# Performance work log

Measured on AMD Instinct MI355X. Metric: run time of the kernel, lower is better.

Reference implementation:

```python
import jax, jax.numpy as jnp
import numpy as np

ROW_PENALTY = 10.0
SENTINEL = 9999.0
T_DIM, D_DIM = 4096, 1024
MASK_DENSITY = 0.7


def setup_inputs() -> dict:
    key = jax.random.key(0)
    k1, k2, k3, k4 = jax.random.split(key, 4)
    X = jax.random.normal(k1, (T_DIM, D_DIM), dtype=jnp.float32)
    H = jax.random.normal(k2, (T_DIM, D_DIM), dtype=jnp.float32)
    C = jax.random.normal(k3, (T_DIM, D_DIM), dtype=jnp.float32)
    # binary observation mask (the torch code treats M as 0/1: M[i]*M[j] > 0)
    M = (jax.random.uniform(k4, (T_DIM, D_DIM)) < MASK_DENSITY).astype(jnp.float32)
    return {"X": X, "H": H, "C": C, "M": M, "T": T_DIM}


def reference(X, H, C, M, T):
    # Binary mask (values already 0/1); M[i]*M[j] > 0  <=>  Mb[i]*Mb[j] == 1.
    Mb = (M > 0).astype(H.dtype)                      # [T, D]
    MH = Mb * H                                       # masked first moment terms
    MH2 = MH * H                                      # masked second moment terms

    # Pairwise masked-variance of (H[i] - H[j]) over dims where both masks are on,
    # expressed exactly as GEMMs (no [T,T,D] intermediate):
    n = Mb @ Mb.T                                     # [T,T] overlap counts
    s1 = MH @ Mb.T - Mb @ MH.T                        # sum_d w * (H_i - H_j)
    s2 = MH2 @ Mb.T - 2.0 * (MH @ MH.T) + Mb @ MH2.T  # sum_d w * (H_i - H_j)^2

    nsafe = jnp.maximum(n, 2.0)
    var = (s2 - s1 * s1 / nsafe) / (nsafe - 1.0)      # unbiased, like torch.var

    am = jnp.argmin(M, axis=1)                        # first-min index per row
    eye = jnp.eye(T, dtype=bool)
    valid = (am[:, None] != am[None, :]) & (~eye) & (n > 1.5)
    scores = jnp.where(valid, var, SENTINEL)          # torch inits scores to 9999

    min_row = jnp.argmin(scores, axis=1)              # [T]
    row_loss = jnp.sum(jnp.linalg.norm(H - H[min_row], axis=1))

    mse = jnp.sum(((X - (H - C)) * M) ** 2)           # MSELoss(reduction='sum') of X*M vs (H-C)*M
    return mse + ROW_PENALTY * row_loss
```

## Files before the change

### kernel.cpp

```cpp
#include <hip/hip_runtime.h>
#include <stdint.h>

#define TD 4096
#define DD 1024
#define SENT 9999.0f

typedef __attribute__((ext_vector_type(4))) float f32x4;
typedef __attribute__((ext_vector_type(8))) short short8;
typedef __attribute__((ext_vector_type(4))) unsigned short ushort4v;

__device__ __forceinline__ unsigned short f2bf(float f) {
  union { float f; unsigned int u; } v; v.f = f;
  unsigned int u = v.u;
  return (unsigned short)((u + 0x7FFFu + ((u >> 16) & 1u)) >> 16);
}

__device__ __forceinline__ void gld_lds16(const void* g, void* l) {
  __builtin_amdgcn_global_load_lds(
      (const __attribute__((address_space(1))) unsigned int*)(size_t)g,
      (__attribute__((address_space(3))) unsigned int*)(unsigned int)(size_t)l,
      16, 0, 0);
}

__global__ __launch_bounds__(256) void k_init(unsigned long long* row_min, float* out) {
  int i = blockIdx.x * 256 + threadIdx.x;
  if (i < TD) row_min[i] = ~0ull;
  if (i == 0) out[0] = 0.0f;
}

__global__ __launch_bounds__(256) void k_prep(
    const float* __restrict__ X, const float* __restrict__ H,
    const float* __restrict__ C, const float* __restrict__ M,
    unsigned short* __restrict__ Mbh, unsigned short* __restrict__ MHh,
    unsigned short* __restrict__ MH2h, int* __restrict__ am,
    float* __restrict__ out)
{
  const int row = blockIdx.x;
  const int tid = threadIdx.x;
  const size_t base = (size_t)row * DD;
  f32x4 x = ((const f32x4*)(X + base))[tid];
  f32x4 h = ((const f32x4*)(H + base))[tid];
  f32x4 c = ((const f32x4*)(C + base))[tid];
  f32x4 m = ((const f32x4*)(M + base))[tid];
  float mse = 0.0f;
  int cand = 0x7FFFFFFF;
  ushort4v mb, mh, mh2;
#pragma unroll
  for (int e = 0; e < 4; ++e) {
    float mv = m[e], hv = h[e];
    float mbv = (mv > 0.0f) ? 1.0f : 0.0f;
    float mhv = mbv * hv;
    float mh2v = mhv * hv;
    mb[e] = f2bf(mbv);
    mh[e] = f2bf(mhv);
    mh2[e] = f2bf(mh2v);
    float t = (x[e] - (hv - c[e])) * mv;
    mse += t * t;
    int d = tid * 4 + e;
    if (mv == 0.0f && d < cand) cand = d;
  }
  *(ushort4v*)(Mbh + base + tid * 4) = mb;
  *(ushort4v*)(MHh + base + tid * 4) = mh;
  *(ushort4v*)(MH2h + base + tid * 4) = mh2;
#pragma unroll
  for (int o = 32; o > 0; o >>= 1) {
    mse += __shfl_down(mse, o);
    int oc = __shfl_down(cand, o);
    cand = (oc < cand) ? oc : cand;
  }
  __shared__ float rs[4];
  __shared__ int ri[4];
  if ((tid & 63) == 0) { rs[tid >> 6] = mse; ri[tid >> 6] = cand; }
  __syncthreads();
  if (tid == 0) {
    float s = rs[0] + rs[1] + rs[2] + rs[3];
    int cm = ri[0];
    cm = (ri[1] < cm) ? ri[1] : cm;
    cm = (ri[2] < cm) ? ri[2] : cm;
    cm = (ri[3] < cm) ? ri[3] : cm;
    atomicAdd(out, s);
    am[row] = (cm == 0x7FFFFFFF) ? 0 : cm;
  }
}

__global__ __launch_bounds__(256, 3) void k_pairvar(
    const unsigned short* __restrict__ Mb, const unsigned short* __restrict__ MH,
    const unsigned short* __restrict__ MH2, const int* __restrict__ am,
    unsigned long long* __restrict__ row_min)
{
  __shared__ unsigned short lds[6 * 64 * 64];
  const int tid = threadIdx.x;
  const int lane = tid & 63;
  const int w = tid >> 6;
  const int wr = w >> 1, wc = w & 1;

  const int kblk = blockIdx.x;
  int bi = (int)((sqrtf(8.0f * (float)kblk + 1.0f) - 1.0f) * 0.5f);
  while ((bi + 1) * (bi + 2) / 2 <= kblk) ++bi;
  while (bi * (bi + 1) / 2 > kblk) --bi;
  const int bj = kblk - bi * (bi + 1) / 2;
  const int i0 = bi * 64, j0 = bj * 64;

  const unsigned short* mats[3] = { Mb, MH, MH2 };
  const int l_row = lane >> 3;
  const int l_ch = lane & 7;
  const int sw_ch = l_ch ^ l_row;

  const unsigned short* gsrc[12];
  unsigned int ldsoff[12];
#pragma unroll
  for (int s = 0; s < 12; ++s) {
    int t = w * 12 + s;
    int tile = t >> 3;
    int rowblk = t & 7;
    int mat = (tile < 3) ? tile : (tile - 3);
    int rbase = (tile < 3) ? i0 : j0;
    int grow = rbase + rowblk * 8 + l_row;
    gsrc[s] = mats[mat] + (size_t)grow * DD + sw_ch * 8;
    ldsoff[s] = (unsigned int)((tile * 4096 + rowblk * 512) * 2);
  }

  f32x4 acc[6][2][2] = {};

  for (int kt = 0; kt < DD / 64; ++kt) {
#pragma unroll
    for (int s = 0; s < 12; ++s)
      gld_lds16(gsrc[s] + kt * 64, (char*)lds + ldsoff[s]);
    __syncthreads();
#pragma unroll
    for (int kc = 0; kc < 2; ++kc) {
      short8 aF[3][2], bF[3][2];
      const int ksub = kc * 4 + (lane >> 4);
#pragma unroll
      for (int m = 0; m < 2; ++m) {
        const int r = wr * 32 + m * 16 + (lane & 15);
        const int sl = ksub ^ (r & 7);
#pragma unroll
        for (int mat = 0; mat < 3; ++mat)
          aF[mat][m] = *(const short8*)&lds[mat * 4096 + r * 64 + sl * 8];
      }
#pragma unroll
      for (int n = 0; n < 2; ++n) {
        const int r = wc * 32 + n * 16 + (lane & 15);
        const int sl = ksub ^ (r & 7);
#pragma unroll
        for (int mat = 0; mat < 3; ++mat)
          bF[mat][n] = *(const short8*)&lds[(3 + mat) * 4096 + r * 64 + sl * 8];
      }
#pragma unroll
      for (int m = 0; m < 2; ++m)
#pragma unroll
        for (int n = 0; n < 2; ++n) {
          acc[0][m][n] = __builtin_amdgcn_mfma_f32_16x16x32_bf16(aF[0][m], bF[0][n], acc[0][m][n], 0, 0, 0);
          acc[1][m][n] = __builtin_amdgcn_mfma_f32_16x16x32_bf16(aF[1][m], bF[0][n], acc[1][m][n], 0, 0, 0);
          acc[2][m][n] = __builtin_amdgcn_mfma_f32_16x16x32_bf16(aF[0][m], bF[1][n], acc[2][m][n], 0, 0, 0);
          acc[3][m][n] = __builtin_amdgcn_mfma_f32_16x16x32_bf16(aF[2][m], bF[0][n], acc[3][m][n], 0, 0, 0);
          acc[4][m][n] = __builtin_amdgcn_mfma_f32_16x16x32_bf16(aF[0][m], bF[2][n], acc[4][m][n], 0, 0, 0);
          acc[5][m][n] = __builtin_amdgcn_mfma_f32_16x16x32_bf16(aF[1][m], bF[1][n], acc[5][m][n], 0, 0, 0);
        }
    }
    __syncthreads();
  }

  const int cl = lane & 15;
  const int lg = lane >> 4;
  int amj[2];
#pragma unroll
  for (int n = 0; n < 2; ++n) amj[n] = am[j0 + wc * 32 + n * 16 + cl];

  unsigned long long bestc[2] = { ~0ull, ~0ull };

#pragma unroll
  for (int m = 0; m < 2; ++m) {
#pragma unroll
    for (int q = 0; q < 4; ++q) {
      const int gi = i0 + wr * 32 + m * 16 + lg * 4 + q;
      const int ami = am[gi];
      unsigned long long best = ~0ull;
#pragma unroll
      for (int n = 0; n < 2; ++n) {
        const int gj = j0 + wc * 32 + n * 16 + cl;
        const float nv = acc[0][m][n][q];
        const float bb = acc[1][m][n][q];
        const float bt = acc[2][m][n][q];
        const float cc = acc[3][m][n][q];
        const float ct = acc[4][m][n][q];
        const float dd = acc[5][m][n][q];
        const float s1 = bb - bt;
        const float s2 = cc - 2.0f * dd + ct;
        const float nsafe = fmaxf(nv, 2.0f);
        const float var = (s2 - s1 * s1 / nsafe) / (nsafe - 1.0f);
        const bool valid = (gi != gj) && (ami != amj[n]) && (nv > 1.5f);
        const float score = valid ? var : SENT;
        unsigned int ub = __float_as_uint(score);
        unsigned int key = (ub & 0x80000000u) ? ~ub : (ub | 0x80000000u);
        unsigned long long pkr = ((unsigned long long)key << 32) | (unsigned int)gj;
        if (pkr < best) best = pkr;
        unsigned long long pkc = ((unsigned long long)key << 32) | (unsigned int)gi;
        if (pkc < bestc[n]) bestc[n] = pkc;
      }
#pragma unroll
      for (int o = 1; o < 16; o <<= 1) {
        unsigned long long other = __shfl_xor(best, o);
        if (other < best) best = other;
      }
      if (cl == 0) atomicMin(&row_min[gi], best);
    }
  }

  if (bi != bj) {
#pragma unroll
    for (int n = 0; n < 2; ++n) {
      unsigned long long b = bestc[n];
      unsigned long long o16 = __shfl_xor(b, 16);
      b = (o16 < b) ? o16 : b;
      unsigned long long o32 = __shfl_xor(b, 32);
      b = (o32 < b) ? o32 : b;
      if (lg == 0) atomicMin(&row_min[j0 + wc * 32 + n * 16 + cl], b);
    }
  }
}

__global__ __launch_bounds__(256) void k_final(
    const float* __restrict__ H, const unsigned long long* __restrict__ row_min,
    float* __restrict__ out)
{
  const int i = blockIdx.x;
  const int tid = threadIdx.x;
  const int j = (int)(unsigned int)(row_min[i] & 0xFFFFFFFFull);
  f32x4 a = ((const f32x4*)(H + (size_t)i * DD))[tid];
  f32x4 b = ((const f32x4*)(H + (size_t)j * DD))[tid];
  float s = 0.0f;
#pragma unroll
  for (int e = 0; e < 4; ++e) {
    float d = a[e] - b[e];
    s += d * d;
  }
#pragma unroll
  for (int o = 32; o > 0; o >>= 1) s += __shfl_down(s, o);
  __shared__ float rs[4];
  if ((tid & 63) == 0) rs[tid >> 6] = s;
  __syncthreads();
  if (tid == 0) {
    float tot = rs[0] + rs[1] + rs[2] + rs[3];
    atomicAdd(out, 10.0f * sqrtf(tot));
  }
}

extern "C" void kernel_launch(void* const* d_in, const int* in_sizes, int n_in,
                              void* d_out, int out_size, void* d_ws, size_t ws_size,
                              hipStream_t stream) {
  const float* X = (const float*)d_in[0];
  const float* H = (const float*)d_in[1];
  const float* C = (const float*)d_in[2];
  const float* M = (const float*)d_in[3];
  float* out = (float*)d_out;

  const size_t SZ = (size_t)TD * DD * sizeof(unsigned short);
  char* ws = (char*)d_ws;
  unsigned short* Mbh = (unsigned short*)(ws);
  unsigned short* MHh = (unsigned short*)(ws + SZ);
  unsigned short* MH2h = (unsigned short*)(ws + 2 * SZ);
  int* am = (int*)(ws + 3 * SZ);
  unsigned long long* row_min = (unsigned long long*)(ws + 3 * SZ + TD * sizeof(int));

  const int NT = TD / 64;
  const int NBLK = NT * (NT + 1) / 2;

  k_init<<<dim3((TD + 255) / 256), dim3(256), 0, stream>>>(row_min, out);
  k_prep<<<dim3(TD), dim3(256), 0, stream>>>(X, H, C, M, Mbh, MHh, MH2h, am, out);
  k_pairvar<<<dim3(NBLK), dim3(256), 0, stream>>>(Mbh, MHh, MH2h, am, row_min);
  k_final<<<dim3(TD), dim3(256), 0, stream>>>(H, row_min, out);
}
```

Baseline: 321.6 us.

## Double-buffer LDS tiles with K=32 steps to overlap global loads with MFMA

Reworks the pairwise-GEMM main loop so each iteration covers K=32 instead of K=64. Two LDS buffers of the same total size are used, and the next tile is prefetched with global_load_lds while MFMAs run on the current one. This cuts the barriers per iteration from two to one and hides global load latency behind compute. The swizzle pattern and the fragment offsets are recomputed for the 32-wide rows. The trade-off is twice as many loop iterations, which may raise the share of bank conflicts and per-iteration overhead.

```diff
diff --git a/kernel.cpp b/kernel.cpp
--- a/kernel.cpp
+++ b/kernel.cpp
@@ -88,7 +88,7 @@
     const unsigned short* __restrict__ MH2, const int* __restrict__ am,
     unsigned long long* __restrict__ row_min)
 {
-  __shared__ unsigned short lds[6 * 64 * 64];
+  __shared__ unsigned short lds[2 * 6 * 64 * 32];
   const int tid = threadIdx.x;
   const int lane = tid & 63;
   const int w = tid >> 6;
@@ -102,67 +102,86 @@
   const int i0 = bi * 64, j0 = bj * 64;
 
   const unsigned short* mats[3] = { Mb, MH, MH2 };
-  const int l_row = lane >> 3;
-  const int l_ch = lane & 7;
-  const int sw_ch = l_ch ^ l_row;
-
-  const unsigned short* gsrc[12];
-  unsigned int ldsoff[12];
-#pragma unroll
-  for (int s = 0; s < 12; ++s) {
-    int t = w * 12 + s;
-    int tile = t >> 3;
-    int rowblk = t & 7;
+
+  const int l_row = lane >> 2;
+  const int l_ch = lane & 3;
+  const int sw_ch = l_ch ^ ((l_row >> 1) & 3);
+
+  const unsigned short* gsrc[6];
+  unsigned int ldsbase[6];
+#pragma unroll
+  for (int s = 0; s < 6; ++s) {
+    int t = w * 6 + s;
+    int tile = t >> 2;
+    int rowblk = t & 3;
     int mat = (tile < 3) ? tile : (tile - 3);
     int rbase = (tile < 3) ? i0 : j0;
-    int grow = rbase + rowblk * 8 + l_row;
+    int grow = rbase + rowblk * 16 + l_row;
     gsrc[s] = mats[mat] + (size_t)grow * DD + sw_ch * 8;
-    ldsoff[s] = (unsigned int)((tile * 4096 + rowblk * 512) * 2);
+    ldsbase[s] = (unsigned int)(tile * 2048 + rowblk * 512);
+  }
+
+  const int cl = lane & 15;
+  const int ksub = lane >> 4;
+  const int sl8 = (ksub ^ ((cl >> 1) & 3)) * 8;
+  int aoff[3][2], boff[3][2];
+#pragma unroll
+  for (int m = 0; m < 2; ++m) {
+    int r = wr * 32 + m * 16 + cl;
+#pragma unroll
+    for (int mat = 0; mat < 3; ++mat)
+      aoff[mat][m] = mat * 2048 + r * 32 + sl8;
+  }
+#pragma unroll
+  for (int n = 0; n < 2; ++n) {
+    int r = wc * 32 + n * 16 + cl;
+#pragma unroll
+    for (int mat = 0; mat < 3; ++mat)
+      boff[mat][n] = (3 + mat) * 2048 + r * 32 + sl8;
   }
 
   f32x4 acc[6][2][2] = {};
 
-  for (int kt = 0; kt < DD / 64; ++kt) {
-#pragma unroll
-    for (int s = 0; s < 12; ++s)
-      gld_lds16(gsrc[s] + kt * 64, (char*)lds + ldsoff[s]);
+#pragma unroll
+  for (int s = 0; s < 6; ++s)
+    gld_lds16(gsrc[s], (char*)lds + (size_t)ldsbase[s] * 2);
+  __syncthreads();
+
+  for (int kt = 0; kt < 32; ++kt) {
+    const int cur = kt & 1;
+    const unsigned int curoff = (unsigned int)cur * 12288u;
+    const unsigned int nxtoff = curoff ^ 12288u;
+    if (kt + 1 < 32) {
+#pragma unroll
+      for (int s = 0; s < 6; ++s)
+        gld_lds16(gsrc[s] + (kt + 1) * 32,
+                  (char*)lds + (size_t)(nxtoff + ldsbase[s]) * 2);
+    }
+    short8 aF[3][2], bF[3][2];
+#pragma unroll
+    for (int m = 0; m < 2; ++m)
+#pragma unroll
+      for (int mat = 0; mat < 3; ++mat)
+        aF[mat][m] = *(const short8*)&lds[curoff + aoff[mat][m]];
+#pragma unroll
+    for (int n = 0; n < 2; ++n)
+#pragma unroll
+      for (int mat = 0; mat < 3; ++mat)
+        bF[mat][n] = *(const short8*)&lds[curoff + boff[mat][n]];
+#pragma unroll
+    for (int m = 0; m < 2; ++m)
+#pragma unroll
+      for (int n = 0; n < 2; ++n) {
+        acc[0][m][n] = __builtin_amdgcn_mfma_f32_16x16x32_bf16(aF[0][m], bF[0][n], acc[0][m][n], 0, 0, 0);
+        acc[1][m][n] = __builtin_amdgcn_mfma_f32_16x16x32_bf16(aF[1][m], bF[0][n], acc[1][m][n], 0, 0, 0);
+        acc[2][m][n] = __builtin_amdgcn_mfma_f32_16x16x32_bf16(aF[0][m], bF[1][n], acc[2][m][n], 0, 0, 0);
+        acc[3][m][n] = __builtin_amdgcn_mfma_f32_16x16x32_bf16(aF[2][m], bF[0][n], acc[3][m][n], 0, 0, 0);
+        acc[4][m][n] = __builtin_amdgcn_mfma_f32_16x16x32_bf16(aF[0][m], bF[2][n], acc[4][m][n], 0, 0, 0);
+        acc[5][m][n] = __builtin_amdgcn_mfma_f32_16x16x32_bf16(aF[1][m], bF[1][n], acc[5][m][n], 0, 0, 0);
+      }
     __syncthreads();
-#pragma unroll
-    for (int kc = 0; kc < 2; ++kc) {
-      short8 aF[3][2], bF[3][2];
-      const int ksub = kc * 4 + (lane >> 4);
-#pragma unroll
-      for (int m = 0; m < 2; ++m) {
-        const int r = wr * 32 + m * 16 + (lane & 15);
-        const int sl = ksub ^ (r & 7);
-#pragma unroll
-        for (int mat = 0; mat < 3; ++mat)
-          aF[mat][m] = *(const short8*)&lds[mat * 4096 + r * 64 + sl * 8];
-      }
-#pragma unroll
-      for (int n = 0; n < 2; ++n) {
-        const int r = wc * 32 + n * 16 + (lane & 15);
-        const int sl = ksub ^ (r & 7);
-#pragma unroll
-        for (int mat = 0; mat < 3; ++mat)
-          bF[mat][n] = *(const short8*)&lds[(3 + mat) * 4096 + r * 64 + sl * 8];
-      }
-#pragma unroll
-      for (int m = 0; m < 2; ++m)
-#pragma unroll
-        for (int n = 0; n < 2; ++n) {
-          acc[0][m][n] = __builtin_amdgcn_mfma_f32_16x16x32_bf16(aF[0][m], bF[0][n], acc[0][m][n], 0, 0, 0);
-          acc[1][m][n] = __builtin_amdgcn_mfma_f32_16x16x32_bf16(aF[1][m], bF[0][n], acc[1][m][n], 0, 0, 0);
-          acc[2][m][n] = __builtin_amdgcn_mfma_f32_16x16x32_bf16(aF[0][m], bF[1][n], acc[2][m][n], 0, 0, 0);
-          acc[3][m][n] = __builtin_amdgcn_mfma_f32_16x16x32_bf16(aF[2][m], bF[0][n], acc[3][m][n], 0, 0, 0);
-          acc[4][m][n] = __builtin_amdgcn_mfma_f32_16x16x32_bf16(aF[0][m], bF[2][n], acc[4][m][n], 0, 0, 0);
-          acc[5][m][n] = __builtin_amdgcn_mfma_f32_16x16x32_bf16(aF[1][m], bF[1][n], acc[5][m][n], 0, 0, 0);
-        }
-    }
-    __syncthreads();
-  }
-
-  const int cl = lane & 15;
+  }
+
   const int lg = lane >> 4;
   int amj[2];
 #pragma unroll
```

Result: slower. 342.5 us (+6.5%).
